# Kernel tuning notes

Hardware: AMD Instinct MI355X
Metric: run time of the kernel (lower is better)

The kernel has to match this reference:

```python
import jax, jax.numpy as jnp
import numpy as np

INPUT_SIZE = 32
HIDDEN_SIZE = 128
N_HEAD = 8
NER_NUMS = 8
D = INPUT_SIZE * NER_NUMS  # 256, attention feature dim per head


def setup_inputs() -> dict:
    key = jax.random.key(0)
    ks = jax.random.split(key, 10)
    B, S = 8, 2048
    x = jax.random.normal(ks[0], (B, S, D), dtype=jnp.float32)
    bi_lstm_o = jax.random.normal(ks[1], (B, S, 2 * HIDDEN_SIZE), dtype=jnp.float32)
    # per-head linear params, stacked on leading head axis (nn.init.normal_ -> std 1)
    Qw = jax.random.normal(ks[2], (N_HEAD, 2 * HIDDEN_SIZE, D), dtype=jnp.float32)
    Qb = jax.random.normal(ks[3], (N_HEAD, D), dtype=jnp.float32)
    Kw = jax.random.normal(ks[4], (N_HEAD, D, D), dtype=jnp.float32)
    Kb = jax.random.normal(ks[5], (N_HEAD, D), dtype=jnp.float32)
    Vw = jax.random.normal(ks[6], (N_HEAD, D, D), dtype=jnp.float32)
    Vb = jax.random.normal(ks[7], (N_HEAD, D), dtype=jnp.float32)
    Cw = jax.random.normal(ks[8], (N_HEAD * D, NER_NUMS), dtype=jnp.float32)
    Cb = jax.random.normal(ks[9], (NER_NUMS,), dtype=jnp.float32)
    return {"x": x, "bi_lstm_o": bi_lstm_o, "Qw": Qw, "Qb": Qb, "Kw": Kw,
            "Kb": Kb, "Vw": Vw, "Vb": Vb, "Cw": Cw, "Cb": Cb}


def reference(x, bi_lstm_o, Qw, Qb, Kw, Kb, Vw, Vb, Cw, Cb):
    # q from bi_lstm_o, k/v from x; all heads batched on axis h
    q = jnp.einsum('bsf,hfd->hbsd', bi_lstm_o, Qw) + Qb[:, None, None, :]
    k = jnp.einsum('bsf,hfd->hbsd', x, Kw) + Kb[:, None, None, :]
    v = jnp.einsum('bsf,hfd->hbsd', x, Vw) + Vb[:, None, None, :]
    scale = 1.0 / jnp.sqrt(jnp.float32(D))
    scores = jnp.einsum('hbsd,hbtd->hbst', q, k) * scale  # [H,B,S,S]
    attn = jax.nn.softmax(scores, axis=-1)
    o = jnp.einsum('hbst,hbtd->hbsd', attn, v)  # [H,B,S,D]
    B, S = x.shape[0], x.shape[1]
    concat = jnp.transpose(o, (1, 2, 0, 3)).reshape(B, S, N_HEAD * D)  # head order matches torch.cat
    return concat @ Cw + Cb
```

## Files before the change

### kernel.cpp

```cpp
#include <hip/hip_runtime.h>

#define H_ 8
#define B_ 8
#define S_ 2048
#define D_ 256

#define KSTRIDE 264
#define VSTRIDE 40
#define QTSTRIDE 136

typedef __attribute__((ext_vector_type(8))) _Float16 half8;
typedef __attribute__((ext_vector_type(4))) _Float16 half4v;
typedef __attribute__((ext_vector_type(2))) _Float16 half2v;
typedef __attribute__((ext_vector_type(4))) float f32x4;

__device__ inline void split8(const float* __restrict__ p, half8& hv, half8& lv) {
  float4 a = *(const float4*)p, b = *(const float4*)(p + 4);
  hv[0] = (_Float16)a.x; hv[1] = (_Float16)a.y; hv[2] = (_Float16)a.z; hv[3] = (_Float16)a.w;
  hv[4] = (_Float16)b.x; hv[5] = (_Float16)b.y; hv[6] = (_Float16)b.z; hv[7] = (_Float16)b.w;
  lv[0] = (_Float16)(a.x - (float)hv[0]); lv[1] = (_Float16)(a.y - (float)hv[1]);
  lv[2] = (_Float16)(a.z - (float)hv[2]); lv[3] = (_Float16)(a.w - (float)hv[3]);
  lv[4] = (_Float16)(b.x - (float)hv[4]); lv[5] = (_Float16)(b.y - (float)hv[5]);
  lv[6] = (_Float16)(b.z - (float)hv[6]); lv[7] = (_Float16)(b.w - (float)hv[7]);
}

__global__ void split_w_kernel(const float* __restrict__ W,
                               _Float16* __restrict__ thi, _Float16* __restrict__ tlo) {
  __shared__ float t[64][65];
  const int h = blockIdx.z, f0 = blockIdx.x * 64, d0 = blockIdx.y * 64;
  const int col = threadIdx.x & 63, rg = threadIdx.x >> 6;
#pragma unroll
  for (int it = 0; it < 16; ++it) {
    int f = rg * 16 + it;
    t[f][col] = W[((size_t)h * 256 + f0 + f) * 256 + d0 + col];
  }
  __syncthreads();
#pragma unroll
  for (int it = 0; it < 16; ++it) {
    int d = rg * 16 + it;
    float v = t[col][d];
    _Float16 hv = (_Float16)v;
    size_t idx = ((size_t)h * 256 + d0 + d) * 256 + f0 + col;
    thi[idx] = hv;
    tlo[idx] = (_Float16)(v - (float)hv);
  }
}

__global__ void out_init_kernel(float* __restrict__ out, const float* __restrict__ Cb) {
  int i = blockIdx.x * blockDim.x + threadIdx.x;
  if (i < B_ * S_ * 8) out[i] = Cb[i & 7];
}

template <int VMODE>
__global__ __launch_bounds__(256, 2) void proj_kernel(
    const float* __restrict__ A,
    const _Float16* __restrict__ Whi, const _Float16* __restrict__ Wlo,
    const float* __restrict__ bias, float oscale, int h0,
    _Float16* __restrict__ Ohi, _Float16* __restrict__ Olo) {
  constexpr bool TMULT = (VMODE != 1);
  __shared__ _Float16 a_hi[128 * VSTRIDE] __attribute__((aligned(16)));
  __shared__ _Float16 b_hi[128 * VSTRIDE] __attribute__((aligned(16)));
  __shared__ _Float16 a_lo[TMULT ? 128 * VSTRIDE : 8] __attribute__((aligned(16)));
  __shared__ _Float16 b_lo[TMULT ? 128 * VSTRIDE : 8] __attribute__((aligned(16)));
  const int tid = threadIdx.x;
  const int w = tid >> 6, lane = tid & 63;
  const int quad = lane >> 4, l15 = lane & 15;
  const int hb = blockIdx.z, h = h0 + (hb >> 3), b = hb & 7;
  const int s0 = blockIdx.x * 128, d0 = blockIdx.y * 128;
  const int wr = w >> 1, wc = w & 1;
  const f32x4 fz = {0.f, 0.f, 0.f, 0.f};
  f32x4 acc[4][4];
#pragma unroll
  for (int i = 0; i < 4; ++i)
#pragma unroll
    for (int j = 0; j < 4; ++j) acc[i][j] = fz;
  const size_t arow0 = (size_t)b * S_ + s0;
  const size_t wrow0 = (size_t)h * 256 + d0;
  for (int kk = 0; kk < 8; ++kk) {
    const int f0 = kk * 32;
    __syncthreads();
#pragma unroll
    for (int i = 0; i < 2; ++i) {
      int cc = i * 256 + tid;
      int r = cc >> 2, ch = (cc & 3) * 8;
      half8 hv, lv;
      split8(A + (arow0 + r) * 256 + f0 + ch, hv, lv);
      *(half8*)&a_hi[r * VSTRIDE + ch] = hv;
      size_t woff = (wrow0 + r) * 256 + f0 + ch;
      *(half8*)&b_hi[r * VSTRIDE + ch] = *(const half8*)(Whi + woff);
      if (TMULT) {
        *(half8*)&a_lo[r * VSTRIDE + ch] = lv;
        *(half8*)&b_lo[r * VSTRIDE + ch] = *(const half8*)(Wlo + woff);
      }
    }
    __syncthreads();
    half8 afh[4], afl[4], bfh[4], bfl[4];
#pragma unroll
    for (int t = 0; t < 4; ++t) {
      int ar = wr * 64 + t * 16 + l15;
      afh[t] = *(const half8*)&a_hi[ar * VSTRIDE + quad * 8];
      int br = wc * 64 + t * 16 + l15;
      bfh[t] = *(const half8*)&b_hi[br * VSTRIDE + quad * 8];
      if (TMULT) {
        afl[t] = *(const half8*)&a_lo[ar * VSTRIDE + quad * 8];
        bfl[t] = *(const half8*)&b_lo[br * VSTRIDE + quad * 8];
      }
    }
#pragma unroll
    for (int rf = 0; rf < 4; ++rf)
#pragma unroll
      for (int cf = 0; cf < 4; ++cf) {
        acc[rf][cf] = __builtin_amdgcn_mfma_f32_16x16x32_f16(afh[rf], bfh[cf], acc[rf][cf], 0, 0, 0);
        if (TMULT) {
          acc[rf][cf] = __builtin_amdgcn_mfma_f32_16x16x32_f16(afh[rf], bfl[cf], acc[rf][cf], 0, 0, 0);
          acc[rf][cf] = __builtin_amdgcn_mfma_f32_16x16x32_f16(afl[rf], bfh[cf], acc[rf][cf], 0, 0, 0);
        }
      }
  }
#pragma unroll
  for (int rf = 0; rf < 4; ++rf) {
#pragma unroll
    for (int cf = 0; cf < 4; ++cf) {
      const int d = d0 + wc * 64 + cf * 16 + l15;
      const float bv = bias[h * 256 + d];
      if (VMODE != 1) {
#pragma unroll
        for (int r = 0; r < 4; ++r) {
          const int s = s0 + wr * 64 + rf * 16 + quad * 4 + r;
          float val = (acc[rf][cf][r] + bv) * oscale;
          _Float16 hvv = (_Float16)val;
          size_t idx = ((size_t)hb * S_ + s) * 256 + d;
          Ohi[idx] = hvv;
          if (VMODE == 0) Olo[idx] = (_Float16)(val - (float)hvv);
        }
      } else {
        half4v pack;
#pragma unroll
        for (int r = 0; r < 4; ++r) pack[r] = (_Float16)((acc[rf][cf][r] + bv) * oscale);
        size_t idx = ((size_t)hb * 256 + d) * S_ + s0 + wr * 64 + rf * 16 + quad * 4;
        *(half4v*)(Ohi + idx) = pack;
      }
    }
  }
}

__global__ __launch_bounds__(256, 2) void flash_kernel(
    const float* __restrict__ bo,
    const _Float16* __restrict__ qwhi, const _Float16* __restrict__ qwlo,
    const float* __restrict__ qbias,
    const _Float16* __restrict__ khi,
    const _Float16* __restrict__ vt, const float* __restrict__ Cw,
    float* __restrict__ out, int h0) {
  __shared__ _Float16 khi_s[32 * KSTRIDE] __attribute__((aligned(16)));
  __shared__ _Float16 vt_s[256 * VSTRIDE] __attribute__((aligned(16)));
  __shared__ _Float16 p_s[4][16 * VSTRIDE] __attribute__((aligned(16)));
  __shared__ _Float16 wbuf[256 * VSTRIDE] __attribute__((aligned(16)));
  const int tid = threadIdx.x, w = tid >> 6, lane = tid & 63;
  const int quad = lane >> 4, l15 = lane & 15;
  const int hb = blockIdx.y, h = h0 + (hb >> 3), b = hb & 7;
  const int qbase = blockIdx.x * 64;
  _Float16* psf = &p_s[0][0];

  const f32x4 fz = {0.f, 0.f, 0.f, 0.f};
  f32x4 qacc[16];
#pragma unroll
  for (int df = 0; df < 16; ++df) qacc[df] = fz;
  for (int kk = 0; kk < 8; ++kk) {
    __syncthreads();
#pragma unroll
    for (int i = 0; i < 4; ++i) {
      int c = i * 256 + tid;
      int dr = c >> 2, ch = (c & 3) * 8;
      size_t woff = ((size_t)h * 256 + dr) * 256 + kk * 32 + ch;
      *(half8*)&vt_s[dr * VSTRIDE + ch] = *(const half8*)(qwhi + woff);
      *(half8*)&wbuf[dr * VSTRIDE + ch] = *(const half8*)(qwlo + woff);
    }
    {
      int rrow = tid >> 2, ch = (tid & 3) * 8;
      half8 hv, lv;
      split8(bo + ((size_t)b * S_ + qbase + rrow) * 256 + kk * 32 + ch, hv, lv);
      *(half8*)&khi_s[rrow * VSTRIDE + ch] = hv;
      *(half8*)&psf[rrow * VSTRIDE + ch] = lv;
    }
    __syncthreads();
    half8 bh = *(const half8*)&khi_s[(w * 16 + l15) * VSTRIDE + quad * 8];
    half8 bl = *(const half8*)&psf[(w * 16 + l15) * VSTRIDE + quad * 8];
#pragma unroll
    for (int df = 0; df < 16; ++df) {
      half8 awh = *(const half8*)&vt_s[(df * 16 + l15) * VSTRIDE + quad * 8];
      half8 awl = *(const half8*)&wbuf[(df * 16 + l15) * VSTRIDE + quad * 8];
      qacc[df] = __builtin_amdgcn_mfma_f32_16x16x32_f16(awh, bh, qacc[df], 0, 0, 0);
      qacc[df] = __builtin_amdgcn_mfma_f32_16x16x32_f16(awl, bh, qacc[df], 0, 0, 0);
      qacc[df] = __builtin_amdgcn_mfma_f32_16x16x32_f16(awh, bl, qacc[df], 0, 0, 0);
    }
  }

  half8 stK[4], stV[4];
  auto LOADKV = [&](int kt) {
    size_t kbase = ((size_t)hb * S_ + (size_t)kt * 32) * 256;
#pragma unroll
    for (int i = 0; i < 4; ++i) {
      int cc = i * 256 + tid;
      int kr = cc >> 5, kch = (cc & 31) * 8;
      stK[i] = *(const half8*)(khi + kbase + kr * 256 + kch);
      int vd = cc >> 2, vch = (cc & 3) * 8;
      stV[i] = *(const half8*)(vt + ((size_t)hb * 256 + vd) * S_ + (size_t)kt * 32 + vch);
    }
  };
  LOADKV(0);

  half8 qfh[8], qfl[8];
#pragma unroll
  for (int ph = 0; ph < 4; ++ph) {
    const int dh = ph >> 1;
    const bool lo = ph & 1;
    __syncthreads();
#pragma unroll
    for (int dfi = 0; dfi < 8; ++dfi) {
      int df = dh * 8 + dfi;
#pragma unroll
      for (int rp = 0; rp < 2; ++rp) {
        half2v hw;
#pragma unroll
        for (int rr2 = 0; rr2 < 2; ++rr2) {
          int r = rp * 2 + rr2;
          float bv = qbias[h * 256 + df * 16 + quad * 4 + r];
          float val = (qacc[df][r] + bv) * 0.0625f;
          _Float16 hv = (_Float16)val;
          hw[rr2] = lo ? (_Float16)(val - (float)hv) : hv;
        }
        *(half2v*)&vt_s[(w * 16 + l15) * QTSTRIDE + dfi * 16 + quad * 4 + rp * 2] = hw;
      }
    }
    __syncthreads();
#pragma unroll
    for (int k2 = 0; k2 < 4; ++k2) {
      half8 v = *(const half8*)&vt_s[(w * 16 + l15) * QTSTRIDE + k2 * 32 + quad * 8];
      if (lo) qfl[dh * 4 + k2] = v;
      else    qfh[dh * 4 + k2] = v;
    }
  }

  f32x4 o_acc[16];
#pragma unroll
  for (int df = 0; df < 16; ++df) o_acc[df] = fz;
  float m_r = -3.0e38f, l_r = 0.f;

  for (int kt = 0; kt < 64; ++kt) {
    __syncthreads();
#pragma unroll
    for (int i = 0; i < 4; ++i) {
      int cc = i * 256 + tid;
      int kr = cc >> 5, kch = (cc & 31) * 8;
      *(half8*)&khi_s[kr * KSTRIDE + kch] = stK[i];
      int vd = cc >> 2, vch = (cc & 3) * 8;
      *(half8*)&vt_s[vd * VSTRIDE + vch] = stV[i];
    }
    __syncthreads();
    if (kt < 63) LOADKV(kt + 1);
    f32x4 sc0 = fz, sc1 = fz;
#pragma unroll
    for (int ks = 0; ks < 8; ++ks) {
      half8 bh0 = *(const half8*)&khi_s[(0 * 16 + l15) * KSTRIDE + ks * 32 + quad * 8];
      sc0 = __builtin_amdgcn_mfma_f32_16x16x32_f16(bh0, qfh[ks], sc0, 0, 0, 0);
      sc0 = __builtin_amdgcn_mfma_f32_16x16x32_f16(bh0, qfl[ks], sc0, 0, 0, 0);
      half8 bh1 = *(const half8*)&khi_s[(1 * 16 + l15) * KSTRIDE + ks * 32 + quad * 8];
      sc1 = __builtin_amdgcn_mfma_f32_16x16x32_f16(bh1, qfh[ks], sc1, 0, 0, 0);
      sc1 = __builtin_amdgcn_mfma_f32_16x16x32_f16(bh1, qfl[ks], sc1, 0, 0, 0);
    }
    float v = fmaxf(fmaxf(fmaxf(sc0[0], sc0[1]), fmaxf(sc0[2], sc0[3])),
                    fmaxf(fmaxf(sc1[0], sc1[1]), fmaxf(sc1[2], sc1[3])));
    v = fmaxf(v, __shfl_xor(v, 16));
    v = fmaxf(v, __shfl_xor(v, 32));
    const float mn = fmaxf(m_r, v);
    const float al = __expf(m_r - mn);
    m_r = mn;
    float p0[4], p1[4], s = 0.f;
#pragma unroll
    for (int r = 0; r < 4; ++r) {
      p0[r] = __expf(sc0[r] - mn);
      p1[r] = __expf(sc1[r] - mn);
      s += p0[r] + p1[r];
    }
    s += __shfl_xor(s, 16);
    s += __shfl_xor(s, 32);
    l_r = l_r * al + s;
    {
      _Float16* pb = &p_s[w][l15 * VSTRIDE + quad * 4];
      half2v w0 = {(_Float16)p0[0], (_Float16)p0[1]};
      half2v w1 = {(_Float16)p0[2], (_Float16)p0[3]};
      half2v w2 = {(_Float16)p1[0], (_Float16)p1[1]};
      half2v w3 = {(_Float16)p1[2], (_Float16)p1[3]};
      *(half2v*)(pb) = w0;
      *(half2v*)(pb + 2) = w1;
      *(half2v*)(pb + 16) = w2;
      *(half2v*)(pb + 18) = w3;
    }
    float al_r[4];
#pragma unroll
    for (int r = 0; r < 4; ++r) al_r[r] = __shfl(al, quad * 4 + r);
#pragma unroll
    for (int df = 0; df < 16; ++df)
#pragma unroll
      for (int r = 0; r < 4; ++r) o_acc[df][r] *= al_r[r];
    __syncthreads();
    half8 pf = *(const half8*)&p_s[w][l15 * VSTRIDE + quad * 8];
#pragma unroll
    for (int df = 0; df < 16; ++df) {
      half8 vf = *(const half8*)&vt_s[(df * 16 + l15) * VSTRIDE + quad * 8];
      o_acc[df] = __builtin_amdgcn_mfma_f32_16x16x32_f16(pf, vf, o_acc[df], 0, 0, 0);
    }
  }
  float rcl[4];
#pragma unroll
  for (int r = 0; r < 4; ++r) rcl[r] = 1.0f / __shfl(l_r, quad * 4 + r);
  float part[32];
#pragma unroll
  for (int i = 0; i < 32; ++i) part[i] = 0.f;
#pragma unroll
  for (int df = 0; df < 16; ++df) {
    const float4* cwv = (const float4*)(Cw + ((size_t)h * 256 + df * 16 + l15) * 8);
    float4 c0 = cwv[0], c1 = cwv[1];
#pragma unroll
    for (int r = 0; r < 4; ++r) {
      float ov = o_acc[df][r] * rcl[r];
      part[r * 8 + 0] += ov * c0.x;
      part[r * 8 + 1] += ov * c0.y;
      part[r * 8 + 2] += ov * c0.z;
      part[r * 8 + 3] += ov * c0.w;
      part[r * 8 + 4] += ov * c1.x;
      part[r * 8 + 5] += ov * c1.y;
      part[r * 8 + 6] += ov * c1.z;
      part[r * 8 + 7] += ov * c1.w;
    }
  }
#pragma unroll
  for (int i = 0; i < 32; ++i) {
    float v = part[i];
    v += __shfl_xor(v, 1);
    v += __shfl_xor(v, 2);
    v += __shfl_xor(v, 4);
    v += __shfl_xor(v, 8);
    part[i] = v;
  }
  if (l15 == 0) {
#pragma unroll
    for (int r = 0; r < 4; ++r) {
      int s = qbase + w * 16 + quad * 4 + r;
#pragma unroll
      for (int j = 0; j < 8; ++j)
        atomicAdd(&out[((size_t)b * S_ + s) * 8 + j], part[r * 8 + j]);
    }
  }
}

extern "C" void kernel_launch(void* const* d_in, const int* in_sizes, int n_in,
                              void* d_out, int out_size, void* d_ws, size_t ws_size,
                              hipStream_t stream) {
  const float* x  = (const float*)d_in[0];
  const float* bo = (const float*)d_in[1];
  const float* Qw = (const float*)d_in[2];
  const float* Qb = (const float*)d_in[3];
  const float* Kw = (const float*)d_in[4];
  const float* Kb = (const float*)d_in[5];
  const float* Vw = (const float*)d_in[6];
  const float* Vb = (const float*)d_in[7];
  const float* Cw = (const float*)d_in[8];
  const float* Cb = (const float*)d_in[9];
  float* out = (float*)d_out;

  const size_t NW  = (size_t)H_ * 256 * 256;
  const size_t NHB = (size_t)B_ * S_ * 256;
  const size_t ALN = 256;
  auto pad = [](size_t b) { return (b + 255) & ~(size_t)255; };

  int HC = 8;
  while (HC > 1) {
    size_t need = 6 * pad(NW * 2) + 2 * pad((size_t)HC * NHB * 2) + ALN;
    if (need <= ws_size) break;
    HC >>= 1;
  }

  char* base = (char*)d_ws;
  size_t off = 0;
  auto carve = [&](size_t nelem) -> _Float16* {
    _Float16* p = (_Float16*)(base + off);
    off += pad(nelem * 2);
    return p;
  };
  _Float16* qwt_hi = carve(NW); _Float16* qwt_lo = carve(NW);
  _Float16* kwt_hi = carve(NW); _Float16* kwt_lo = carve(NW);
  _Float16* vwt_hi = carve(NW); _Float16* vwt_lo = carve(NW);
  const size_t NC = (size_t)HC * NHB;
  _Float16* k_hi = carve(NC);
  _Float16* v_t  = carve(NC);

  dim3 wg(4, 4, 8);
  split_w_kernel<<<wg, 256, 0, stream>>>(Qw, qwt_hi, qwt_lo);
  split_w_kernel<<<wg, 256, 0, stream>>>(Kw, kwt_hi, kwt_lo);
  split_w_kernel<<<wg, 256, 0, stream>>>(Vw, vwt_hi, vwt_lo);
  out_init_kernel<<<(B_ * S_ * 8) / 256, 256, 0, stream>>>(out, Cb);

  for (int h0 = 0; h0 < H_; h0 += HC) {
    dim3 pg(16, 2, HC * 8);
    proj_kernel<2><<<pg, 256, 0, stream>>>(x, kwt_hi, kwt_lo, Kb, 1.0f, h0, k_hi, nullptr);
    proj_kernel<1><<<pg, 256, 0, stream>>>(x, vwt_hi, vwt_lo, Vb, 1.0f, h0, v_t, nullptr);
    dim3 fg(32, HC * 8);
    flash_kernel<<<fg, 256, 0, stream>>>(bo, qwt_hi, qwt_lo, Qb, k_hi, v_t, Cw, out, h0);
  }
}
```

Measured before the change: 843.9 us.

## Pass softmax probabilities via lane shuffles and skip rescaling below a max threshold

Replaces the shared-memory round trip for the P tile (store, __syncthreads, reload) with register packing and cross-lane shuffles that build the MFMA A operand directly. This removes a block barrier and LDS traffic from every key tile. It also adds lazy online-softmax rescaling: the running max and the o_acc rescale are updated only when some lane's new max exceeds the old one by more than 8, so most iterations skip the 64-element multiply. Exponents can then reach up to e^8 before rescaling, which relies on fp16 P values staying in range, and the freed p_s scratch is moved into khi_s.

```diff
diff --git a/kernel.cpp b/kernel.cpp
--- a/kernel.cpp
+++ b/kernel.cpp
@@ -144,6 +144,11 @@
   }
 }
 
+__device__ inline unsigned int pack2(float a, float b) {
+  half2v h; h[0] = (_Float16)a; h[1] = (_Float16)b;
+  return __builtin_bit_cast(unsigned int, h);
+}
+
 __global__ __launch_bounds__(256, 2) void flash_kernel(
     const float* __restrict__ bo,
     const _Float16* __restrict__ qwhi, const _Float16* __restrict__ qwlo,
@@ -153,13 +158,11 @@
     float* __restrict__ out, int h0) {
   __shared__ _Float16 khi_s[32 * KSTRIDE] __attribute__((aligned(16)));
   __shared__ _Float16 vt_s[256 * VSTRIDE] __attribute__((aligned(16)));
-  __shared__ _Float16 p_s[4][16 * VSTRIDE] __attribute__((aligned(16)));
   __shared__ _Float16 wbuf[256 * VSTRIDE] __attribute__((aligned(16)));
   const int tid = threadIdx.x, w = tid >> 6, lane = tid & 63;
   const int quad = lane >> 4, l15 = lane & 15;
   const int hb = blockIdx.y, h = h0 + (hb >> 3), b = hb & 7;
   const int qbase = blockIdx.x * 64;
-  _Float16* psf = &p_s[0][0];
 
   const f32x4 fz = {0.f, 0.f, 0.f, 0.f};
   f32x4 qacc[16];
@@ -180,11 +183,11 @@
       half8 hv, lv;
       split8(bo + ((size_t)b * S_ + qbase + rrow) * 256 + kk * 32 + ch, hv, lv);
       *(half8*)&khi_s[rrow * VSTRIDE + ch] = hv;
-      *(half8*)&psf[rrow * VSTRIDE + ch] = lv;
+      *(half8*)&khi_s[2560 + rrow * VSTRIDE + ch] = lv;
     }
     __syncthreads();
     half8 bh = *(const half8*)&khi_s[(w * 16 + l15) * VSTRIDE + quad * 8];
-    half8 bl = *(const half8*)&psf[(w * 16 + l15) * VSTRIDE + quad * 8];
+    half8 bl = *(const half8*)&khi_s[2560 + (w * 16 + l15) * VSTRIDE + quad * 8];
 #pragma unroll
     for (int df = 0; df < 16; ++df) {
       half8 awh = *(const half8*)&vt_s[(df * 16 + l15) * VSTRIDE + quad * 8];
@@ -272,43 +275,50 @@
                     fmaxf(fmaxf(sc1[0], sc1[1]), fmaxf(sc1[2], sc1[3])));
     v = fmaxf(v, __shfl_xor(v, 16));
     v = fmaxf(v, __shfl_xor(v, 32));
-    const float mn = fmaxf(m_r, v);
-    const float al = __expf(m_r - mn);
-    m_r = mn;
+    if (__any(v > m_r + 8.0f)) {
+      const float mn = fmaxf(m_r, v);
+      const float al = __expf(m_r - mn);
+      m_r = mn;
+      l_r *= al;
+      float al_r[4];
+#pragma unroll
+      for (int r = 0; r < 4; ++r) al_r[r] = __shfl(al, quad * 4 + r);
+#pragma unroll
+      for (int df = 0; df < 16; ++df)
+#pragma unroll
+        for (int r = 0; r < 4; ++r) o_acc[df][r] *= al_r[r];
+    }
     float p0[4], p1[4], s = 0.f;
 #pragma unroll
     for (int r = 0; r < 4; ++r) {
-      p0[r] = __expf(sc0[r] - mn);
-      p1[r] = __expf(sc1[r] - mn);
+      p0[r] = __expf(sc0[r] - m_r);
+      p1[r] = __expf(sc1[r] - m_r);
       s += p0[r] + p1[r];
     }
     s += __shfl_xor(s, 16);
     s += __shfl_xor(s, 32);
-    l_r = l_r * al + s;
+    l_r += s;
     {
-      _Float16* pb = &p_s[w][l15 * VSTRIDE + quad * 4];
-      half2v w0 = {(_Float16)p0[0], (_Float16)p0[1]};
-      half2v w1 = {(_Float16)p0[2], (_Float16)p0[3]};
-      half2v w2 = {(_Float16)p1[0], (_Float16)p1[1]};
-      half2v w3 = {(_Float16)p1[2], (_Float16)p1[3]};
-      *(half2v*)(pb) = w0;
-      *(half2v*)(pb + 2) = w1;
-      *(half2v*)(pb + 16) = w2;
-      *(half2v*)(pb + 18) = w3;
-    }
-    float al_r[4];
-#pragma unroll
-    for (int r = 0; r < 4; ++r) al_r[r] = __shfl(al, quad * 4 + r);
-#pragma unroll
-    for (int df = 0; df < 16; ++df)
-#pragma unroll
-      for (int r = 0; r < 4; ++r) o_acc[df][r] *= al_r[r];
-    __syncthreads();
-    half8 pf = *(const half8*)&p_s[w][l15 * VSTRIDE + quad * 8];
-#pragma unroll
-    for (int df = 0; df < 16; ++df) {
-      half8 vf = *(const half8*)&vt_s[(df * 16 + l15) * VSTRIDE + quad * 8];
-      o_acc[df] = __builtin_amdgcn_mfma_f32_16x16x32_f16(pf, vf, o_acc[df], 0, 0, 0);
+      unsigned int u0 = pack2(p0[0], p0[1]), u1 = pack2(p0[2], p0[3]);
+      unsigned int v0 = pack2(p1[0], p1[1]), v1 = pack2(p1[2], p1[3]);
+      const int src0 = ((quad & 1) << 5) + l15;
+      const int src1 = src0 + 16;
+      unsigned int a0 = __shfl(u0, src0), a1 = __shfl(u1, src0);
+      unsigned int a2 = __shfl(u0, src1), a3 = __shfl(u1, src1);
+      unsigned int c0 = __shfl(v0, src0), c1 = __shfl(v1, src0);
+      unsigned int c2 = __shfl(v0, src1), c3 = __shfl(v1, src1);
+      union U { unsigned int u[4]; half8 h; } pu;
+      const bool hiq = quad >= 2;
+      pu.u[0] = hiq ? c0 : a0;
+      pu.u[1] = hiq ? c1 : a1;
+      pu.u[2] = hiq ? c2 : a2;
+      pu.u[3] = hiq ? c3 : a3;
+      half8 pf = pu.h;
+#pragma unroll
+      for (int df = 0; df < 16; ++df) {
+        half8 vf = *(const half8*)&vt_s[(df * 16 + l15) * VSTRIDE + quad * 8];
+        o_acc[df] = __builtin_amdgcn_mfma_f32_16x16x32_f16(pf, vf, o_acc[df], 0, 0, 0);
+      }
     }
   }
   float rcl[4];
```

New measurement: 777.9 us. 7.8% less time.
